# Optimization experiments

Hardware: AMD Instinct MI355X
Metric: run time of the kernel (lower is better)

The kernel has to match this reference:

```python
import jax, jax.numpy as jnp
import numpy as np
import math

B, N, EPG = 128, 512, 8192            # graphs, nodes/graph, edges/graph
E = B * EPG
DIN, H, DOUT = 128, 128, 10
RATIO = 0.8
K1 = math.ceil(RATIO * N)             # 410 nodes/graph after pool 1
K2 = math.ceil(RATIO * K1)            # 328 nodes/graph after pool 2
EPS = 1e-5


def setup_inputs() -> dict:
    key = jax.random.key(0)
    ks = jax.random.split(key, 16)
    x = jax.random.normal(ks[0], (B * N, DIN), jnp.float32)
    gid = jnp.repeat(jnp.arange(B, dtype=jnp.int32), EPG)
    src = jax.random.randint(ks[1], (E,), 0, N, dtype=jnp.int32) + gid * N
    dst = jax.random.randint(ks[2], (E,), 0, N, dtype=jnp.int32) + gid * N
    edge_index = jnp.stack([src, dst])

    def w(k, shape, fan_in):
        return jax.random.uniform(k, shape, jnp.float32, -1.0, 1.0) / np.sqrt(fan_in).astype(np.float32)

    return {
        "x": x, "edge_index": edge_index,
        "conv1_W": w(ks[3], (DIN, H), DIN), "conv1_b": jnp.zeros((H,), jnp.float32),
        "conv2_W": w(ks[4], (H, H), H),     "conv2_b": jnp.zeros((H,), jnp.float32),
        "score1_W": w(ks[5], (H, 1), H),    "score1_b": jnp.zeros((1,), jnp.float32),
        "score2_W": w(ks[6], (H, 1), H),    "score2_b": jnp.zeros((1,), jnp.float32),
        "bn1_g": jnp.ones((H,), jnp.float32), "bn1_b": jnp.zeros((H,), jnp.float32),
        "bn1_m": 0.1 * jax.random.normal(ks[7], (H,), jnp.float32),
        "bn1_v": jax.random.uniform(ks[8], (H,), jnp.float32, 0.5, 1.5),
        "bn2_g": jnp.ones((H,), jnp.float32), "bn2_b": jnp.zeros((H,), jnp.float32),
        "bn2_m": 0.1 * jax.random.normal(ks[9], (H,), jnp.float32),
        "bn2_v": jax.random.uniform(ks[10], (H,), jnp.float32, 0.5, 1.5),
        "lin0_W": w(ks[11], (DOUT, DIN), DIN), "lin0_b": jnp.zeros((DOUT,), jnp.float32),
        "lin1_W": w(ks[12], (DOUT, H), H),     "lin1_b": jnp.zeros((DOUT,), jnp.float32),
        "lin2_W": w(ks[13], (DOUT, H), H),     "lin2_b": jnp.zeros((DOUT,), jnp.float32),
    }


def gcn(h_in, src, dst, emask, W, b, n):
    # PyG GCNConv: self-loops + symmetric normalization D^-1/2 (A+I) D^-1/2 (XW) + b
    deg = jnp.ones((n,), h_in.dtype).at[dst].add(emask)      # self-loop counts as 1
    dinv = jax.lax.rsqrt(deg)
    coef = (dinv[src] * dinv[dst] * emask)[:, None]          # masked-out edges -> 0
    h = h_in @ W
    agg = jnp.zeros_like(h).at[dst].add(h[src] * coef)
    return agg + h * (dinv * dinv)[:, None] + b              # self-loop message + bias


def sag_pool(x, score, src, dst, emask, n_per, k):
    # topk per graph (equal-sized graphs -> static shapes), x <- x[perm]*tanh(score[perm])
    idx = jax.lax.top_k(score.reshape(B, n_per), k)[1]                      # [B,k]
    perm = (idx.astype(jnp.int32) + (jnp.arange(B, dtype=jnp.int32) * n_per)[:, None]).reshape(-1)
    xn = x[perm] * jnp.tanh(score[perm])[:, None]
    # filter_adj: remap surviving nodes, mask edges touching dropped nodes
    remap = jnp.full((B * n_per,), -1, jnp.int32).at[perm].set(jnp.arange(B * k, dtype=jnp.int32))
    s2, d2 = remap[src], remap[dst]
    em2 = emask * (s2 >= 0).astype(emask.dtype) * (d2 >= 0).astype(emask.dtype)
    return xn, jnp.maximum(s2, 0), jnp.maximum(d2, 0), em2


def bn_relu(x, g, b, m, v):
    # eval-mode BatchNorm1d followed by ReLU
    return jax.nn.relu(g * (x - m) * jax.lax.rsqrt(v + EPS) + b)


def reference(x, edge_index, conv1_W, conv1_b, conv2_W, conv2_b,
              score1_W, score1_b, score2_W, score2_b,
              bn1_g, bn1_b, bn1_m, bn1_v, bn2_g, bn2_b, bn2_m, bn2_v,
              lin0_W, lin0_b, lin1_W, lin1_b, lin2_W, lin2_b):
    src, dst = edge_index[0], edge_index[1]
    emask = jnp.ones((E,), x.dtype)
    hidden = [(x, N)]
    # layer 0: GCNConv -> SAGPool -> BN -> ReLU
    h = gcn(x, src, dst, emask, conv1_W, conv1_b, B * N)
    s = gcn(h, src, dst, emask, score1_W, score1_b, B * N)[:, 0]
    h, src, dst, emask = sag_pool(h, s, src, dst, emask, N, K1)
    h = bn_relu(h, bn1_g, bn1_b, bn1_m, bn1_v)
    hidden.append((h, K1))
    # layer 1
    h = gcn(h, src, dst, emask, conv2_W, conv2_b, B * K1)
    s = gcn(h, src, dst, emask, score2_W, score2_b, B * K1)[:, 0]
    h, src, dst, emask = sag_pool(h, s, src, dst, emask, K1, K2)
    h = bn_relu(h, bn2_g, bn2_b, bn2_m, bn2_v)
    hidden.append((h, K2))
    # jumping-knowledge readout: global_add_pool each rep, per-layer linear, sum (dropout eval = id)
    lins = [(lin0_W, lin0_b), (lin1_W, lin1_b), (lin2_W, lin2_b)]
    out = jnp.zeros((B, DOUT), x.dtype)
    for (hh, n_per), (W, bb) in zip(hidden, lins):
        pooled = hh.reshape(B, n_per, -1).sum(axis=1)   # global_add_pool (segment sum)
        out = out + pooled @ W.T + bb
    return out
```

## Files before the change

### kernel.cpp

```cpp
#include <hip/hip_runtime.h>

#define Bg   128
#define NPG  512
#define EPGc 8192
#define Etot (Bg*EPGc)
#define DOUTc 10
#define K1c  410
#define K2c  328
#define N0c  (Bg*NPG)
#define N1c  (Bg*K1c)
#define N2c  (Bg*K2c)
#define EPSc 1e-5f

typedef __attribute__((ext_vector_type(8))) short s8v;
typedef __attribute__((ext_vector_type(4))) float f4v;

static __device__ __forceinline__ unsigned short bf_rne(float x) {
  unsigned u = __float_as_uint(x);
  u += 0x7FFFu + ((u >> 16) & 1u);
  return (unsigned short)(u >> 16);
}
static __device__ __forceinline__ float bf_f(unsigned short h) {
  return __uint_as_float(((unsigned)h) << 16);
}

static __global__ void k_packW(const float* __restrict__ W1,
                               const float* __restrict__ W2,
                               unsigned short* __restrict__ pk) {
  int i = blockIdx.x * 256 + threadIdx.x;
  if (i >= 32768) return;
  const float* W = (i < 16384) ? W1 : W2;
  unsigned short* d = pk + ((i < 16384) ? 0 : 32768);
  int ii = i & 16383;
  int grp = ii >> 9, lane = (ii >> 3) & 63, j = ii & 7;
  int kk = grp >> 3, t = grp & 7;
  int k = kk * 32 + (lane >> 4) * 8 + j;
  int n = t * 16 + (lane & 15);
  float w = W[k * 128 + n];
  unsigned short hi = bf_rne(w);
  d[ii] = hi;
  d[16384 + ii] = bf_rne(w - bf_f(hi));
}

static __global__ __launch_bounds__(512) void k_prep0(const int* __restrict__ src,
                                                      const int* __restrict__ dst,
                                                      const float* __restrict__ x,
                                                      float* __restrict__ dinv,
                                                      int* __restrict__ rp,
                                                      int2* __restrict__ e2,
                                                      float* __restrict__ pooled) {
  __shared__ int    cnt[NPG];
  __shared__ float  sdv[NPG];
  __shared__ int    srp[NPG];
  __shared__ int    sbuf[512];
  __shared__ float4 xred[512];
  int g = blockIdx.x, tid = threadIdx.x;
  cnt[tid] = 0;
  if (tid < 128) {
    pooled[Bg * 128 + g * 128 + tid] = 0.f;
    pooled[2 * Bg * 128 + g * 128 + tid] = 0.f;
  }
  {
    int c4 = tid & 31, rq = tid >> 5;
    float4 a = make_float4(0.f, 0.f, 0.f, 0.f);
    const float4* xp = (const float4*)(x + (size_t)g * NPG * 128);
    for (int r = rq; r < NPG; r += 16) {
      float4 v = xp[r * 32 + c4];
      a.x += v.x; a.y += v.y; a.z += v.z; a.w += v.w;
    }
    xred[tid] = a;
  }
  __syncthreads();
  if (tid < 32) {
    float4 a = make_float4(0.f, 0.f, 0.f, 0.f);
    for (int q = 0; q < 16; ++q) {
      float4 v = xred[q * 32 + tid];
      a.x += v.x; a.y += v.y; a.z += v.z; a.w += v.w;
    }
    ((float4*)&pooled[g * 128])[tid] = a;
  }
  const int* sp = src + (size_t)g * EPGc;
  const int* dp = dst + (size_t)g * EPGc;
  for (int e = tid; e < EPGc; e += 512) atomicAdd(&cnt[dp[e] - g * NPG], 1);
  __syncthreads();
  int c = cnt[tid];
  float dv = 1.0f / sqrtf(1.0f + (float)c);
  sdv[tid] = dv;
  dinv[g * NPG + tid] = dv;
  sbuf[tid] = c;
  __syncthreads();
  for (int off = 1; off < 512; off <<= 1) {
    int t = (tid >= off) ? sbuf[tid - off] : 0;
    __syncthreads();
    sbuf[tid] += t;
    __syncthreads();
  }
  srp[tid] = sbuf[tid] - c;
  rp[g * (NPG + 1) + tid] = sbuf[tid] - c;
  if (tid == 511) rp[g * (NPG + 1) + NPG] = sbuf[511];
  cnt[tid] = 0;
  __syncthreads();
  for (int e = tid; e < EPGc; e += 512) {
    int s = sp[e], d = dp[e];
    int dl = d - g * NPG;
    int pos = srp[dl] + atomicAdd(&cnt[dl], 1);
    e2[(size_t)g * EPGc + pos] =
        make_int2(s, __float_as_int(sdv[s - g * NPG] * sdv[dl]));
  }
}

static __global__ __launch_bounds__(256) void k_gemm3(const float* __restrict__ X,
                                                      const unsigned short* __restrict__ pk,
                                                      float* __restrict__ Y) {
  __shared__ unsigned short wl[32768];
  int tid = threadIdx.x;
  for (int i = tid; i < 4096; i += 256) ((int4*)wl)[i] = ((const int4*)pk)[i];
  int wv = tid >> 6, lane = tid & 63;
  int q = lane >> 4, m16 = lane & 15;
  size_t row = (size_t)blockIdx.x * 64 + wv * 16 + m16;
  s8v ahi[4], alo[4];
#pragma unroll
  for (int kk = 0; kk < 4; ++kk) {
    const float* xr = X + row * 128 + kk * 32 + q * 8;
    float4 a0 = *(const float4*)xr;
    float4 a1 = *(const float4*)(xr + 4);
    float av[8] = {a0.x, a0.y, a0.z, a0.w, a1.x, a1.y, a1.z, a1.w};
    union { unsigned short u[8]; s8v v; } H, L;
#pragma unroll
    for (int j = 0; j < 8; ++j) {
      unsigned short h = bf_rne(av[j]);
      H.u[j] = h;
      L.u[j] = bf_rne(av[j] - bf_f(h));
    }
    ahi[kk] = H.v; alo[kk] = L.v;
  }
  __syncthreads();
  int orow0 = blockIdx.x * 64 + wv * 16 + q * 4;
#pragma unroll
  for (int t = 0; t < 8; ++t) {
    f4v acc = {0.f, 0.f, 0.f, 0.f};
#pragma unroll
    for (int kk = 0; kk < 4; ++kk) {
      s8v bhi = *(const s8v*)&wl[(kk * 8 + t) * 512 + lane * 8];
      s8v blo = *(const s8v*)&wl[16384 + (kk * 8 + t) * 512 + lane * 8];
      acc = __builtin_amdgcn_mfma_f32_16x16x32_bf16(ahi[kk], bhi, acc, 0, 0, 0);
      acc = __builtin_amdgcn_mfma_f32_16x16x32_bf16(alo[kk], bhi, acc, 0, 0, 0);
      acc = __builtin_amdgcn_mfma_f32_16x16x32_bf16(ahi[kk], blo, acc, 0, 0, 0);
    }
#pragma unroll
    for (int r = 0; r < 4; ++r)
      Y[(size_t)(orow0 + r) * 128 + t * 16 + m16] = acc[r];
  }
}

template <int NPER, int RG>
static __global__ __launch_bounds__(256) void k_agg3(const float* __restrict__ h0,
                                                     const float* __restrict__ dinv,
                                                     const float* __restrict__ bias,
                                                     const int* __restrict__ rp,
                                                     const int2* __restrict__ e2,
                                                     const float* __restrict__ sw,
                                                     float* __restrict__ h1,
                                                     float* __restrict__ spre) {
  int tid = threadIdx.x;
  int hw = tid >> 5, l = tid & 31;
  int b = blockIdx.x;
  int xcd = b & 7, slot = b >> 3;
  int g = xcd * 16 + (slot & 15);
  int rowgrp = slot >> 4;
  int li = rowgrp * 8 + hw;
  if (li >= NPER) return;
  int j = g * NPER + li;
  const int* rpg = rp + g * (NPER + 1);
  int start = rpg[li], end = rpg[li + 1];
  const int2* ep = e2 + (size_t)g * EPGc;
  float di = dinv[j];
  float sc = di * di;
  float4 acc = *(const float4*)&h0[(size_t)j * 128 + l * 4];
  float4 bb = ((const float4*)bias)[l];
  acc.x = acc.x * sc + bb.x; acc.y = acc.y * sc + bb.y;
  acc.z = acc.z * sc + bb.z; acc.w = acc.w * sc + bb.w;
  int e = start;
  for (; e + 8 <= end; e += 8) {
    int2 p[8];
#pragma unroll
    for (int qq = 0; qq < 8; ++qq) p[qq] = ep[e + qq];
    float4 v[8];
#pragma unroll
    for (int qq = 0; qq < 8; ++qq) v[qq] = *(const float4*)&h0[(size_t)p[qq].x * 128 + l * 4];
#pragma unroll
    for (int qq = 0; qq < 8; ++qq) {
      float c = __int_as_float(p[qq].y);
      acc.x += v[qq].x * c; acc.y += v[qq].y * c;
      acc.z += v[qq].z * c; acc.w += v[qq].w * c;
    }
  }
  for (; e + 4 <= end; e += 4) {
    int2 p0 = ep[e], p1 = ep[e + 1], p2 = ep[e + 2], p3 = ep[e + 3];
    float4 v0 = *(const float4*)&h0[(size_t)p0.x * 128 + l * 4];
    float4 v1 = *(const float4*)&h0[(size_t)p1.x * 128 + l * 4];
    float4 v2 = *(const float4*)&h0[(size_t)p2.x * 128 + l * 4];
    float4 v3 = *(const float4*)&h0[(size_t)p3.x * 128 + l * 4];
    float c0 = __int_as_float(p0.y), c1 = __int_as_float(p1.y);
    float c2 = __int_as_float(p2.y), c3 = __int_as_float(p3.y);
    acc.x += v0.x * c0 + v1.x * c1 + v2.x * c2 + v3.x * c3;
    acc.y += v0.y * c0 + v1.y * c1 + v2.y * c2 + v3.y * c3;
    acc.z += v0.z * c0 + v1.z * c1 + v2.z * c2 + v3.z * c3;
    acc.w += v0.w * c0 + v1.w * c1 + v2.w * c2 + v3.w * c3;
  }
  for (; e < end; ++e) {
    int2 pp = ep[e];
    float c = __int_as_float(pp.y);
    float4 v = *(const float4*)&h0[(size_t)pp.x * 128 + l * 4];
    acc.x += v.x * c; acc.y += v.y * c; acc.z += v.z * c; acc.w += v.w * c;
  }
  ((float4*)&h1[(size_t)j * 128])[l] = acc;
  float4 w4 = ((const float4*)sw)[l];
  float pr = acc.x * w4.x + acc.y * w4.y + acc.z * w4.z + acc.w * w4.w;
#pragma unroll
  for (int off = 16; off; off >>= 1) pr += __shfl_xor(pr, off, 64);
  if (l == 0) spre[j] = pr;
}

template <int NPER>
static __global__ void k_score2(const float* __restrict__ spre, const float* __restrict__ dinv,
                                const float* __restrict__ bptr, const int* __restrict__ rp,
                                const int2* __restrict__ e2, float* __restrict__ s, int n) {
  int j = blockIdx.x * 256 + threadIdx.x;
  if (j >= n) return;
  int g = j / NPER, li = j - g * NPER;
  const int* rpg = rp + g * (NPER + 1);
  int start = rpg[li], end = rpg[li + 1];
  const int2* ep = e2 + (size_t)g * EPGc;
  float di = dinv[j];
  float acc = spre[j] * di * di + bptr[0];
  int e = start;
  for (; e + 4 <= end; e += 4) {
    int2 p0 = ep[e], p1 = ep[e + 1], p2 = ep[e + 2], p3 = ep[e + 3];
    float a0 = spre[p0.x], a1 = spre[p1.x], a2 = spre[p2.x], a3 = spre[p3.x];
    acc += a0 * __int_as_float(p0.y) + a1 * __int_as_float(p1.y) +
           a2 * __int_as_float(p2.y) + a3 * __int_as_float(p3.y);
  }
  for (; e < end; ++e) { int2 pp = ep[e]; acc += spre[pp.x] * __int_as_float(pp.y); }
  s[j] = acc;
}

template <int NPER, int K>
static __global__ __launch_bounds__(512) void k_repool(const float* __restrict__ sv,
                                                       const int* __restrict__ src,
                                                       const int* __restrict__ dst,
                                                       int* __restrict__ perm,
                                                       float* __restrict__ dinv2,
                                                       int* __restrict__ rp2,
                                                       int2* __restrict__ e2) {
  __shared__ float sc[512];
  __shared__ int   sidx[512];
  __shared__ short rmp[NPER];
  __shared__ int   cnt[K];
  __shared__ float sdv[K];
  __shared__ int   srp[K];
  __shared__ int   sbuf[512];
  int g = blockIdx.x, tid = threadIdx.x;
  sc[tid] = (tid < NPER) ? sv[g * NPER + tid] : -3.402823466e38f;
  sidx[tid] = tid;
  if (tid < NPER) rmp[tid] = -1;
  __syncthreads();
  for (int kk = 2; kk <= 512; kk <<= 1) {
    for (int j = kk >> 1; j > 0; j >>= 1) {
      int i = tid, p = i ^ j;
      if (p > i) {
        bool up = ((i & kk) == 0);
        float si = sc[i], sp2 = sc[p];
        if (up ? (si < sp2) : (si > sp2)) {
          sc[i] = sp2; sc[p] = si;
          int t = sidx[i]; sidx[i] = sidx[p]; sidx[p] = t;
        }
      }
      __syncthreads();
    }
  }
  if (tid < K) {
    perm[g * K + tid] = g * NPER + sidx[tid];
    rmp[sidx[tid]] = (short)tid;
    cnt[tid] = 0;
  }
  __syncthreads();
  const int* sp = src + (size_t)g * EPGc;
  const int* dp = dst + (size_t)g * EPGc;
  for (int e = tid; e < EPGc; e += 512) {
    int s = rmp[sp[e] - g * NPER];
    int d = rmp[dp[e] - g * NPER];
    if ((s | d) >= 0) atomicAdd(&cnt[d], 1);
  }
  __syncthreads();
  int c = (tid < K) ? cnt[tid] : 0;
  if (tid < K) {
    float dv = 1.0f / sqrtf(1.0f + (float)c);
    sdv[tid] = dv;
    dinv2[g * K + tid] = dv;
  }
  sbuf[tid] = c;
  __syncthreads();
  for (int off = 1; off < 512; off <<= 1) {
    int t = (tid >= off) ? sbuf[tid - off] : 0;
    __syncthreads();
    sbuf[tid] += t;
    __syncthreads();
  }
  if (tid < K) { srp[tid] = sbuf[tid] - c; rp2[g * (K + 1) + tid] = sbuf[tid] - c; cnt[tid] = 0; }
  if (tid == 511) rp2[g * (K + 1) + K] = sbuf[511];
  __syncthreads();
  for (int e = tid; e < EPGc; e += 512) {
    int s = rmp[sp[e] - g * NPER];
    int d = rmp[dp[e] - g * NPER];
    if ((s | d) >= 0) {
      int pos = srp[d] + atomicAdd(&cnt[d], 1);
      e2[(size_t)g * EPGc + pos] = make_int2(g * K + s, __float_as_int(sdv[s] * sdv[d]));
    }
  }
}

template <int NPER, int K>
static __global__ __launch_bounds__(256) void k_topk(const float* __restrict__ s,
                                                     int* __restrict__ perm) {
  __shared__ float sc[512];
  __shared__ int   idx[512];
  int g = blockIdx.x, tid = threadIdx.x;
  for (int i = tid; i < 512; i += 256) {
    if (i < NPER) { sc[i] = s[g * NPER + i]; idx[i] = i; }
    else          { sc[i] = -3.402823466e38f; idx[i] = 0; }
  }
  __syncthreads();
  for (int kk = 2; kk <= 512; kk <<= 1) {
    for (int j = kk >> 1; j > 0; j >>= 1) {
      for (int base = 0; base < 512; base += 256) {
        int i = base + tid;
        int p = i ^ j;
        if (p > i) {
          bool up = ((i & kk) == 0);
          float si = sc[i], sp = sc[p];
          if (up ? (si < sp) : (si > sp)) {
            sc[i] = sp; sc[p] = si;
            int t = idx[i]; idx[i] = idx[p]; idx[p] = t;
          }
        }
      }
      __syncthreads();
    }
  }
  for (int r = tid; r < K; r += 256) perm[g * K + r] = g * NPER + idx[r];
}

template <int NPER, int CH, bool WXP>
static __global__ __launch_bounds__(128) void k_poolbn(const float* __restrict__ h,
                                                       const float* __restrict__ s,
                                                       const int* __restrict__ perm,
                                                       const float* __restrict__ gg,
                                                       const float* __restrict__ bb,
                                                       const float* __restrict__ mm,
                                                       const float* __restrict__ vv,
                                                       float* __restrict__ xp,
                                                       float* __restrict__ pooledseg) {
  int g = blockIdx.x / CH, cidx = blockIdx.x - g * CH;
  int f = threadIdx.x;
  const int rows = (NPER + CH - 1) / CH;
  int r0 = cidx * rows, r1 = min(NPER, r0 + rows);
  float G = gg[f], Bb = bb[f], Mm = mm[f];
  float inv = 1.0f / sqrtf(vv[f] + EPSc);
  float acc = 0.f;
  for (int r = r0; r < r1; ++r) {
    int j = g * NPER + r;
    int old = perm[j];
    float t = tanhf(s[old]);
    float val = h[(size_t)old * 128 + f] * t;
    float o = fmaxf(G * (val - Mm) * inv + Bb, 0.f);
    if (WXP) xp[(size_t)j * 128 + f] = o;
    acc += o;
  }
  atomicAdd(&pooledseg[g * 128 + f], acc);
}

static __global__ void k_final(const float* __restrict__ pooled,
                               const float* __restrict__ w0, const float* __restrict__ b0,
                               const float* __restrict__ w1, const float* __restrict__ b1,
                               const float* __restrict__ w2, const float* __restrict__ b2,
                               float* __restrict__ out) {
  int t = blockIdx.x * 256 + threadIdx.x;
  if (t >= Bg * DOUTc) return;
  int g = t / DOUTc, o = t - g * DOUTc;
  const float* p0 = pooled + g * 128;
  const float* p1 = pooled + Bg * 128 + g * 128;
  const float* p2 = pooled + 2 * Bg * 128 + g * 128;
  float acc = b0[o] + b1[o] + b2[o];
  for (int k = 0; k < 128; ++k)
    acc += p0[k] * w0[o * 128 + k] + p1[k] * w1[o * 128 + k] + p2[k] * w2[o * 128 + k];
  out[t] = acc;
}

extern "C" void kernel_launch(void* const* d_in, const int* in_sizes, int n_in,
                              void* d_out, int out_size, void* d_ws, size_t ws_size,
                              hipStream_t stream) {
  (void)in_sizes; (void)n_in; (void)out_size; (void)ws_size;
  const float* x    = (const float*)d_in[0];
  const int*   ei   = (const int*)d_in[1];
  const int*   src0 = ei;
  const int*   dst0 = ei + Etot;
  const float* c1W = (const float*)d_in[2];  const float* c1b = (const float*)d_in[3];
  const float* c2W = (const float*)d_in[4];  const float* c2b = (const float*)d_in[5];
  const float* s1W = (const float*)d_in[6];  const float* s1b = (const float*)d_in[7];
  const float* s2W = (const float*)d_in[8];  const float* s2b = (const float*)d_in[9];
  const float* bn1g = (const float*)d_in[10]; const float* bn1b = (const float*)d_in[11];
  const float* bn1m = (const float*)d_in[12]; const float* bn1v = (const float*)d_in[13];
  const float* bn2g = (const float*)d_in[14]; const float* bn2b = (const float*)d_in[15];
  const float* bn2m = (const float*)d_in[16]; const float* bn2v = (const float*)d_in[17];
  const float* l0W = (const float*)d_in[18]; const float* l0b = (const float*)d_in[19];
  const float* l1W = (const float*)d_in[20]; const float* l1b = (const float*)d_in[21];
  const float* l2W = (const float*)d_in[22]; const float* l2b = (const float*)d_in[23];
  float* out = (float*)d_out;

  char* p = (char*)d_ws;
  auto alloc = [&](size_t bytes) { char* q = p; p += (bytes + 255) & ~(size_t)255; return q; };
  float* h0    = (float*)alloc((size_t)N0c * 128 * 4);
  float* h1    = (float*)alloc((size_t)N0c * 128 * 4);
  float* xp1   = (float*)alloc((size_t)N1c * 128 * 4);
  float* dinv  = (float*)alloc((size_t)N0c * 4);
  float* dinv2 = (float*)alloc((size_t)N1c * 4);
  int*   rp    = (int*)alloc((size_t)Bg * (NPG + 1) * 4);
  int*   rp2   = (int*)alloc((size_t)Bg * (K1c + 1) * 4);
  int2*  e2    = (int2*)alloc((size_t)Etot * 8);
  float* spre  = (float*)alloc((size_t)N0c * 4);
  float* sv    = (float*)alloc((size_t)N0c * 4);
  int*   perm  = (int*)alloc((size_t)N1c * 4);
  unsigned short* pk = (unsigned short*)alloc((size_t)65536 * 2);
  float* pooled= (float*)alloc((size_t)3 * Bg * 128 * 4);

  dim3 b256(256), b512(512), b128(128);

  k_packW<<<128, b256, 0, stream>>>(c1W, c2W, pk);
  k_prep0<<<Bg, b512, 0, stream>>>(src0, dst0, x, dinv, rp, e2, pooled);
  k_gemm3<<<N0c / 64, b256, 0, stream>>>(x, pk, h0);
  k_agg3<NPG, 64><<<128 * 64, b256, 0, stream>>>(h0, dinv, c1b, rp, e2, s1W, h1, spre);
  k_score2<NPG><<<(N0c + 255) / 256, b256, 0, stream>>>(spre, dinv, s1b, rp, e2, sv, N0c);
  k_repool<NPG, K1c><<<Bg, b512, 0, stream>>>(sv, src0, dst0, perm, dinv2, rp2, e2);
  k_poolbn<K1c, 8, true><<<Bg * 8, b128, 0, stream>>>(h1, sv, perm, bn1g, bn1b, bn1m, bn1v,
                                                      xp1, pooled + Bg * 128);

  float* g1 = h0;
  float* h2 = h1;
  k_gemm3<<<N1c / 64, b256, 0, stream>>>(xp1, pk + 32768, g1);
  k_agg3<K1c, 52><<<128 * 52, b256, 0, stream>>>(g1, dinv2, c2b, rp2, e2, s2W, h2, spre);
  k_score2<K1c><<<(N1c + 255) / 256, b256, 0, stream>>>(spre, dinv2, s2b, rp2, e2, sv, N1c);
  k_topk<K1c, K2c><<<Bg, b256, 0, stream>>>(sv, perm);
  k_poolbn<K2c, 8, false><<<Bg * 8, b128, 0, stream>>>(h2, sv, perm, bn2g, bn2b, bn2m, bn2v,
                                                       nullptr, pooled + 2 * Bg * 128);

  k_final<<<(Bg * DOUTc + 255) / 256, b256, 0, stream>>>(pooled, l0W, l0b, l1W, l1b, l2W, l2b, out);
}
```

Measured before the change: 385.1 us.

## Fold weight packing into prep kernel, split x-sum, retune gather unrolls and poolbn grid

Weight packing moves into the per-graph prep kernel, so one launch goes away. The global sum of x moves out of prep into a separate k_xsum kernel that reduces with atomics over 2048 small blocks. The 8-way unrolled gather is removed from the feature aggregation and added to the scalar score aggregation instead. The pool+BN kernels now split each graph into 16 chunks instead of 8, with an early exit for empty chunks. The aim is to shorten the serial prep kernel and raise parallelism, at the cost of an extra launch and more atomics.

```diff
diff --git a/kernel.cpp b/kernel.cpp
--- a/kernel.cpp
+++ b/kernel.cpp
@@ -24,27 +24,11 @@
   return __uint_as_float(((unsigned)h) << 16);
 }
 
-static __global__ void k_packW(const float* __restrict__ W1,
-                               const float* __restrict__ W2,
-                               unsigned short* __restrict__ pk) {
-  int i = blockIdx.x * 256 + threadIdx.x;
-  if (i >= 32768) return;
-  const float* W = (i < 16384) ? W1 : W2;
-  unsigned short* d = pk + ((i < 16384) ? 0 : 32768);
-  int ii = i & 16383;
-  int grp = ii >> 9, lane = (ii >> 3) & 63, j = ii & 7;
-  int kk = grp >> 3, t = grp & 7;
-  int k = kk * 32 + (lane >> 4) * 8 + j;
-  int n = t * 16 + (lane & 15);
-  float w = W[k * 128 + n];
-  unsigned short hi = bf_rne(w);
-  d[ii] = hi;
-  d[16384 + ii] = bf_rne(w - bf_f(hi));
-}
-
 static __global__ __launch_bounds__(512) void k_prep0(const int* __restrict__ src,
                                                       const int* __restrict__ dst,
-                                                      const float* __restrict__ x,
+                                                      const float* __restrict__ W1,
+                                                      const float* __restrict__ W2,
+                                                      unsigned short* __restrict__ pk,
                                                       float* __restrict__ dinv,
                                                       int* __restrict__ rp,
                                                       int2* __restrict__ e2,
@@ -53,32 +37,28 @@
   __shared__ float  sdv[NPG];
   __shared__ int    srp[NPG];
   __shared__ int    sbuf[512];
-  __shared__ float4 xred[512];
   int g = blockIdx.x, tid = threadIdx.x;
   cnt[tid] = 0;
   if (tid < 128) {
+    pooled[g * 128 + tid] = 0.f;
     pooled[Bg * 128 + g * 128 + tid] = 0.f;
     pooled[2 * Bg * 128 + g * 128 + tid] = 0.f;
   }
-  {
-    int c4 = tid & 31, rq = tid >> 5;
-    float4 a = make_float4(0.f, 0.f, 0.f, 0.f);
-    const float4* xp = (const float4*)(x + (size_t)g * NPG * 128);
-    for (int r = rq; r < NPG; r += 16) {
-      float4 v = xp[r * 32 + c4];
-      a.x += v.x; a.y += v.y; a.z += v.z; a.w += v.w;
-    }
-    xred[tid] = a;
-  }
-  __syncthreads();
-  if (tid < 32) {
-    float4 a = make_float4(0.f, 0.f, 0.f, 0.f);
-    for (int q = 0; q < 16; ++q) {
-      float4 v = xred[q * 32 + tid];
-      a.x += v.x; a.y += v.y; a.z += v.z; a.w += v.w;
-    }
-    ((float4*)&pooled[g * 128])[tid] = a;
-  }
+  if (tid < 256) {
+    int i = g * 256 + tid;
+    const float* W = (i < 16384) ? W1 : W2;
+    unsigned short* d = pk + ((i < 16384) ? 0 : 32768);
+    int ii = i & 16383;
+    int grp = ii >> 9, lane = (ii >> 3) & 63, j = ii & 7;
+    int kk = grp >> 3, t = grp & 7;
+    int k = kk * 32 + (lane >> 4) * 8 + j;
+    int n = t * 16 + (lane & 15);
+    float w = W[k * 128 + n];
+    unsigned short hi = bf_rne(w);
+    d[ii] = hi;
+    d[16384 + ii] = bf_rne(w - bf_f(hi));
+  }
+  __syncthreads();
   const int* sp = src + (size_t)g * EPGc;
   const int* dp = dst + (size_t)g * EPGc;
   for (int e = tid; e < EPGc; e += 512) atomicAdd(&cnt[dp[e] - g * NPG], 1);
@@ -107,6 +87,16 @@
     e2[(size_t)g * EPGc + pos] =
         make_int2(s, __float_as_int(sdv[s - g * NPG] * sdv[dl]));
   }
+}
+
+static __global__ __launch_bounds__(128) void k_xsum(const float* __restrict__ x,
+                                                     float* __restrict__ pooled0) {
+  int g = blockIdx.x >> 4, c = blockIdx.x & 15;
+  int f = threadIdx.x;
+  float acc = 0.f;
+  const float* p = x + ((size_t)g * NPG + c * 32) * 128 + f;
+  for (int i = 0; i < 32; ++i, p += 128) acc += *p;
+  atomicAdd(&pooled0[g * 128 + f], acc);
 }
 
 static __global__ __launch_bounds__(256) void k_gemm3(const float* __restrict__ X,
@@ -181,20 +171,6 @@
   acc.x = acc.x * sc + bb.x; acc.y = acc.y * sc + bb.y;
   acc.z = acc.z * sc + bb.z; acc.w = acc.w * sc + bb.w;
   int e = start;
-  for (; e + 8 <= end; e += 8) {
-    int2 p[8];
-#pragma unroll
-    for (int qq = 0; qq < 8; ++qq) p[qq] = ep[e + qq];
-    float4 v[8];
-#pragma unroll
-    for (int qq = 0; qq < 8; ++qq) v[qq] = *(const float4*)&h0[(size_t)p[qq].x * 128 + l * 4];
-#pragma unroll
-    for (int qq = 0; qq < 8; ++qq) {
-      float c = __int_as_float(p[qq].y);
-      acc.x += v[qq].x * c; acc.y += v[qq].y * c;
-      acc.z += v[qq].z * c; acc.w += v[qq].w * c;
-    }
-  }
   for (; e + 4 <= end; e += 4) {
     int2 p0 = ep[e], p1 = ep[e + 1], p2 = ep[e + 2], p3 = ep[e + 3];
     float4 v0 = *(const float4*)&h0[(size_t)p0.x * 128 + l * 4];
@@ -235,6 +211,16 @@
   float di = dinv[j];
   float acc = spre[j] * di * di + bptr[0];
   int e = start;
+  for (; e + 8 <= end; e += 8) {
+    int2 p[8];
+#pragma unroll
+    for (int q = 0; q < 8; ++q) p[q] = ep[e + q];
+    float a[8];
+#pragma unroll
+    for (int q = 0; q < 8; ++q) a[q] = spre[p[q].x];
+#pragma unroll
+    for (int q = 0; q < 8; ++q) acc += a[q] * __int_as_float(p[q].y);
+  }
   for (; e + 4 <= end; e += 4) {
     int2 p0 = ep[e], p1 = ep[e + 1], p2 = ep[e + 2], p3 = ep[e + 3];
     float a0 = spre[p0.x], a1 = spre[p1.x], a2 = spre[p2.x], a3 = spre[p3.x];
@@ -365,6 +351,7 @@
   int f = threadIdx.x;
   const int rows = (NPER + CH - 1) / CH;
   int r0 = cidx * rows, r1 = min(NPER, r0 + rows);
+  if (r0 >= r1) return;
   float G = gg[f], Bb = bb[f], Mm = mm[f];
   float inv = 1.0f / sqrtf(vv[f] + EPSc);
   float acc = 0.f;
@@ -436,14 +423,14 @@
 
   dim3 b256(256), b512(512), b128(128);
 
-  k_packW<<<128, b256, 0, stream>>>(c1W, c2W, pk);
-  k_prep0<<<Bg, b512, 0, stream>>>(src0, dst0, x, dinv, rp, e2, pooled);
+  k_prep0<<<Bg, b512, 0, stream>>>(src0, dst0, c1W, c2W, pk, dinv, rp, e2, pooled);
+  k_xsum<<<Bg * 16, b128, 0, stream>>>(x, pooled);
   k_gemm3<<<N0c / 64, b256, 0, stream>>>(x, pk, h0);
   k_agg3<NPG, 64><<<128 * 64, b256, 0, stream>>>(h0, dinv, c1b, rp, e2, s1W, h1, spre);
   k_score2<NPG><<<(N0c + 255) / 256, b256, 0, stream>>>(spre, dinv, s1b, rp, e2, sv, N0c);
   k_repool<NPG, K1c><<<Bg, b512, 0, stream>>>(sv, src0, dst0, perm, dinv2, rp2, e2);
-  k_poolbn<K1c, 8, true><<<Bg * 8, b128, 0, stream>>>(h1, sv, perm, bn1g, bn1b, bn1m, bn1v,
-                                                      xp1, pooled + Bg * 128);
+  k_poolbn<K1c, 16, true><<<Bg * 16, b128, 0, stream>>>(h1, sv, perm, bn1g, bn1b, bn1m, bn1v,
+                                                        xp1, pooled + Bg * 128);
 
   float* g1 = h0;
   float* h2 = h1;
@@ -451,8 +438,8 @@
   k_agg3<K1c, 52><<<128 * 52, b256, 0, stream>>>(g1, dinv2, c2b, rp2, e2, s2W, h2, spre);
   k_score2<K1c><<<(N1c + 255) / 256, b256, 0, stream>>>(spre, dinv2, s2b, rp2, e2, sv, N1c);
   k_topk<K1c, K2c><<<Bg, b256, 0, stream>>>(sv, perm);
-  k_poolbn<K2c, 8, false><<<Bg * 8, b128, 0, stream>>>(h2, sv, perm, bn2g, bn2b, bn2m, bn2v,
-                                                       nullptr, pooled + 2 * Bg * 128);
+  k_poolbn<K2c, 16, false><<<Bg * 16, b128, 0, stream>>>(h2, sv, perm, bn2g, bn2b, bn2m, bn2v,
+                                                         nullptr, pooled + 2 * Bg * 128);
 
   k_final<<<(Bg * DOUTc + 255) / 256, b256, 0, stream>>>(pooled, l0W, l0b, l1W, l1b, l2W, l2b, out);
 }
```

After: 339.7 us. 1.13x faster.
